# Kernel optimization log

Measured on AMD Instinct MI355X. Metric: run time of the kernel, lower is better.

Reference implementation:

```python
import jax, jax.numpy as jnp
import numpy as np

N, NFEAT, NHID, NCLASS = 384, 512, 192, 64


def setup_inputs() -> dict:
    key = jax.random.key(0)
    ks = jax.random.split(key, 16)
    s = 0.05
    inp = {
        "x": jax.random.normal(ks[0], (N, NFEAT), jnp.float32),
        # normalized dense adjacency surrogates (row-scaled so outputs stay O(1))
        "adj": jax.random.uniform(ks[1], (N, N), jnp.float32) / N,
        "adj1": jax.random.uniform(ks[2], (N, N * N), jnp.float32) / (N * N),
        # nn.Linear emb / cls
        "W_emb": jax.random.normal(ks[3], (NFEAT, NHID), jnp.float32) * s,
        "b_emb": jnp.zeros((NHID,), jnp.float32),
        "W_cls": jax.random.normal(ks[4], (NHID, NCLASS), jnp.float32) * s,
        "b_cls": jnp.zeros((NCLASS,), jnp.float32),
        # GraphConvolution gc1, gc2
        "W1": jax.random.normal(ks[5], (NHID, NHID), jnp.float32) * s,
        "b1": jnp.zeros((NHID,), jnp.float32),
        "W2": jax.random.normal(ks[6], (NHID, NHID), jnp.float32) * s,
        "b2": jnp.zeros((NHID,), jnp.float32),
        # GraphConvolution_edge gc_e, gc_e2
        "We": jax.random.normal(ks[7], (NHID, NHID), jnp.float32) * s,
        "be": jnp.zeros((NHID,), jnp.float32),
        "We2": jax.random.normal(ks[8], (NHID, NHID), jnp.float32) * s,
        "be2": jnp.zeros((NHID,), jnp.float32),
    }
    return inp


def _outer_edge(a, b):
    # [N,H] x [N,H] -> [N*N, H] elementwise outer-product edge features
    n, h = a.shape
    return (a[:, None, :] * b[None, :, :]).reshape(n * n, h)


def reference(x, adj, adj1, W_emb, b_emb, W_cls, b_cls, W1, b1, W2, b2, We, be, We2, be2):
    # eval mode: dropout is identity
    x_init = x @ W_emb + b_emb                      # [N,H]
    edge_feat = _outer_edge(x_init, x_init)          # [N*N,H]
    # gc_e: adj1 @ (edge_feat @ We) + be
    x_e = jax.nn.relu(adj1 @ (edge_feat @ We) + be)  # [N,H]
    # gc1: adj @ (x_init @ W1) + b1
    x1 = jax.nn.relu(adj @ (x_init @ W1) + b1)       # [N,H]
    xs = x1 + x_e + x_init
    x_mid = adj @ (xs @ W2) + b2                     # gc2
    edge_feat1 = _outer_edge(x1, x1)                 # [N*N,H]
    x_e2 = adj1 @ ((edge_feat + edge_feat1) @ We2) + be2  # gc_e2
    h = jax.nn.relu(x_mid + x_e2)
    logits = h @ W_cls + b_cls                       # [N,C]
    return jax.nn.log_softmax(logits, axis=1)
```

## Files before the change

### kernel.cpp

```cpp
#include <hip/hip_runtime.h>

#define NN 384
#define NF 512
#define NH 192
#define NC 64

typedef __bf16 bf16x8 __attribute__((ext_vector_type(8)));
typedef float f32x4 __attribute__((ext_vector_type(4)));

static __device__ __forceinline__ float b2f(unsigned short u) {
  union { unsigned int i; float f; } v; v.i = ((unsigned int)u) << 16; return v.f;
}
static __device__ __forceinline__ unsigned short f2b(float f) {
  unsigned int u = __float_as_uint(f);
  unsigned int r = (u + 0x7FFFu + ((u >> 16) & 1u)) >> 16;
  return (unsigned short)r;
}

__global__ void __launch_bounds__(192) k_emb(
    const float* __restrict__ x, const float* __restrict__ W_emb,
    const float* __restrict__ b_emb, const float* __restrict__ W1,
    float* __restrict__ xinit, float* __restrict__ t1,
    unsigned short* __restrict__ uT)
{
  __shared__ float xl[4][NF];
  __shared__ float xi[4][NH];
  const int r0 = blockIdx.x * 4;
  const int tid = threadIdx.x;
#pragma unroll
  for (int rr = 0; rr < 4; ++rr)
    for (int k = tid; k < NF; k += 192)
      xl[rr][k] = x[(size_t)(r0 + rr) * NF + k];
  __syncthreads();
  const int h = tid;
  float a0 = b_emb[h], a1 = a0, a2 = a0, a3 = a0;
  for (int k = 0; k < NF; ++k) {
    float w = W_emb[k * NH + h];
    a0 += xl[0][k] * w; a1 += xl[1][k] * w; a2 += xl[2][k] * w; a3 += xl[3][k] * w;
  }
  float acc[4] = {a0, a1, a2, a3};
#pragma unroll
  for (int rr = 0; rr < 4; ++rr) {
    xinit[(r0 + rr) * NH + h] = acc[rr];
    xi[rr][h] = acc[rr];
    uT[h * NN + (r0 + rr)] = f2b(acc[rr]);
  }
  __syncthreads();
  float c0 = 0.f, c1 = 0.f, c2 = 0.f, c3 = 0.f;
  for (int k = 0; k < NH; ++k) {
    float w = W1[k * NH + h];
    c0 += xi[0][k] * w; c1 += xi[1][k] * w; c2 += xi[2][k] * w; c3 += xi[3][k] * w;
  }
  t1[(r0 + 0) * NH + h] = c0;
  t1[(r0 + 1) * NH + h] = c1;
  t1[(r0 + 2) * NH + h] = c2;
  t1[(r0 + 3) * NH + h] = c3;
}

__global__ void __launch_bounds__(192) k_gc1(
    const float* __restrict__ adj, const float* __restrict__ t1,
    const float* __restrict__ b1, float* __restrict__ x1,
    unsigned short* __restrict__ vT)
{
  __shared__ float al[4][NN];
  const int r0 = blockIdx.x * 4;
  const int tid = threadIdx.x;
#pragma unroll
  for (int rr = 0; rr < 4; ++rr)
    for (int j = tid; j < NN; j += 192)
      al[rr][j] = adj[(size_t)(r0 + rr) * NN + j];
  __syncthreads();
  const int h = tid;
  float a0 = b1[h], a1 = a0, a2 = a0, a3 = a0;
  for (int j = 0; j < NN; ++j) {
    float t = t1[j * NH + h];
    a0 += al[0][j] * t; a1 += al[1][j] * t; a2 += al[2][j] * t; a3 += al[3][j] * t;
  }
  float acc[4] = {a0, a1, a2, a3};
#pragma unroll
  for (int rr = 0; rr < 4; ++rr) {
    float v = fmaxf(acc[rr], 0.f);
    x1[(r0 + rr) * NH + h] = v;
    vT[h * NN + (r0 + rr)] = f2b(v);
  }
}

__global__ void __launch_bounds__(512, 2) k_edge(
    const float* __restrict__ adj1, const unsigned short* __restrict__ uT,
    const unsigned short* __restrict__ vT,
    float* __restrict__ E0p, float* __restrict__ E1p)
{
  __shared__ __align__(16) unsigned char lds_raw[81920];
  float* Af = (float*)lds_raw;
  unsigned short* Bf = (unsigned short*)(lds_raw + 32768);

  const int tid = threadIdx.x;
  const int wv = tid >> 6, l = tid & 63;
  const int lr = l & 15, lg = l >> 4;
  const int rg = wv >> 2, hg = (wv >> 1) & 1, uv = wv & 1;
  const int bid = blockIdx.x;
  const int r = bid / 3, ig = bid - r * 3;
  const int i0 = ig * 128;
  const float* __restrict__ Ar = adj1 + (size_t)r * (NN * NN);

  const int aunit = (l & 7) ^ (l >> 3);
  const int bunit = (l & 3) ^ ((l >> 3) & 3);

  f32x4 acc[4][6];
  const f32x4 zero = {0.f, 0.f, 0.f, 0.f};
#pragma unroll
  for (int s = 0; s < 4; ++s)
#pragma unroll
    for (int t = 0; t < 6; ++t) acc[s][t] = zero;

  auto STAGE = [&](int buf, int kb) {
#pragma unroll
    for (int p = 0; p < 2; ++p) {
      const int rowbase = wv * 16 + p * 8;
      const float* g = Ar + (size_t)(i0 + rowbase + (l >> 3)) * NN + kb + 4 * aunit;
      __builtin_amdgcn_global_load_lds(
          (const __attribute__((address_space(1))) unsigned int*)g,
          (__attribute__((address_space(3))) unsigned int*)(Af + buf * 4096 + rowbase * 32),
          16, 0, 0);
    }
#pragma unroll
    for (int q = 0; q < 3; ++q) {
      const int m = wv * 3 + q;
      const int uvs = (m >= 12) ? 1 : 0;
      const int H0 = (m - uvs * 12) * 16;
      const unsigned short* src =
          (uvs ? vT : uT) + (H0 + (l >> 2)) * NN + kb + 8 * bunit;
      __builtin_amdgcn_global_load_lds(
          (const __attribute__((address_space(1))) unsigned int*)src,
          (__attribute__((address_space(3))) unsigned int*)(Bf + buf * 12288 + uvs * 6144 + H0 * 32),
          16, 0, 0);
    }
  };

  STAGE(0, 0);
  __syncthreads();

  const unsigned short* selT = uv ? vT : uT;
  int buf = 0;
  for (int kk = 0; kk < 12; ++kk) {
    if (kk < 11) STAGE(buf ^ 1, (kk + 1) * 32);

    const float* Ab = Af + buf * 4096;
    const unsigned short* Bb = Bf + buf * 12288 + uv * 6144;

    bf16x8 bfr[6];
#pragma unroll
    for (int t = 0; t < 6; ++t) {
      const int h = (hg * 6 + t) * 16 + lr;
      bfr[t] = *reinterpret_cast<const bf16x8*>(Bb + h * 32 + 8 * (lg ^ ((lr >> 1) & 3)));
    }
#pragma unroll
    for (int s = 0; s < 4; ++s) {
      const int R = rg * 64 + s * 16 + lr;
      const float* rowp = Ab + R * 32;
      f32x4 q0 = *reinterpret_cast<const f32x4*>(rowp + 4 * ((2 * lg) ^ (lr & 7)));
      f32x4 q1 = *reinterpret_cast<const f32x4*>(rowp + 4 * (((2 * lg) + 1) ^ (lr & 7)));
      bf16x8 af;
      af[0] = (__bf16)q0[0]; af[1] = (__bf16)q0[1];
      af[2] = (__bf16)q0[2]; af[3] = (__bf16)q0[3];
      af[4] = (__bf16)q1[0]; af[5] = (__bf16)q1[1];
      af[6] = (__bf16)q1[2]; af[7] = (__bf16)q1[3];
#pragma unroll
      for (int t = 0; t < 6; ++t)
        acc[s][t] = __builtin_amdgcn_mfma_f32_16x16x32_bf16(af, bfr[t], acc[s][t], 0, 0, 0);
    }
    __syncthreads();
    buf ^= 1;
  }

  float e[6];
#pragma unroll
  for (int t = 0; t < 6; ++t) {
    const int h = (hg * 6 + t) * 16 + lr;
    float ac = 0.f;
#pragma unroll
    for (int s = 0; s < 4; ++s) {
      const int ii = i0 + rg * 64 + s * 16 + lg * 4;
      ushort4 w4 = *reinterpret_cast<const ushort4*>(selT + h * NN + ii);
      ac += b2f(w4.x) * acc[s][t][0] + b2f(w4.y) * acc[s][t][1]
          + b2f(w4.z) * acc[s][t][2] + b2f(w4.w) * acc[s][t][3];
    }
    ac += __shfl_xor(ac, 16);
    ac += __shfl_xor(ac, 32);
    e[t] = ac;
  }
  float* scratch = (float*)lds_raw;
  if (rg == 1 && lg == 0) {
#pragma unroll
    for (int t = 0; t < 6; ++t)
      scratch[uv * 192 + (hg * 6 + t) * 16 + lr] = e[t];
  }
  __syncthreads();
  if (rg == 0 && lg == 0) {
    float* Ep = uv ? E1p : E0p;
#pragma unroll
    for (int t = 0; t < 6; ++t) {
      const int h = (hg * 6 + t) * 16 + lr;
      Ep[((size_t)ig * NN + r) * NH + h] = e[t] + scratch[uv * 192 + h];
    }
  }
}

__global__ void __launch_bounds__(192) k_mid(
    const float* __restrict__ E0p, const float* __restrict__ E1p,
    const float* __restrict__ x1, const float* __restrict__ xinit,
    const float* __restrict__ We, const float* __restrict__ be,
    const float* __restrict__ W2, const float* __restrict__ We2,
    const float* __restrict__ be2, float* __restrict__ t2,
    float* __restrict__ xe2)
{
  __shared__ float e0l[4][NH], s01[4][NH], xsl[4][NH];
  const int r0 = blockIdx.x * 4;
  const int h = threadIdx.x;
#pragma unroll
  for (int rr = 0; rr < 4; ++rr) {
    const int idx = (r0 + rr) * NH + h;
    float e0v = E0p[idx] + E0p[NN * NH + idx] + E0p[2 * NN * NH + idx];
    float e1v = E1p[idx] + E1p[NN * NH + idx] + E1p[2 * NN * NH + idx];
    e0l[rr][h] = e0v;
    s01[rr][h] = e0v + e1v;
  }
  __syncthreads();
  float x0 = be[h], x1a = x0, x2 = x0, x3 = x0;
  for (int k = 0; k < NH; ++k) {
    float w = We[k * NH + h];
    x0 += e0l[0][k] * w; x1a += e0l[1][k] * w; x2 += e0l[2][k] * w; x3 += e0l[3][k] * w;
  }
  float xe[4] = {x0, x1a, x2, x3};
#pragma unroll
  for (int rr = 0; rr < 4; ++rr) {
    const int idx = (r0 + rr) * NH + h;
    xsl[rr][h] = fmaxf(xe[rr], 0.f) + x1[idx] + xinit[idx];
  }
  __syncthreads();
  float t0 = 0.f, t1v = 0.f, t2v = 0.f, t3 = 0.f;
  float b0 = be2[h], b1v = b0, b2v = b0, b3 = b0;
  for (int k = 0; k < NH; ++k) {
    float w2 = W2[k * NH + h];
    float w3 = We2[k * NH + h];
    t0 += xsl[0][k] * w2; t1v += xsl[1][k] * w2; t2v += xsl[2][k] * w2; t3 += xsl[3][k] * w2;
    b0 += s01[0][k] * w3; b1v += s01[1][k] * w3; b2v += s01[2][k] * w3; b3 += s01[3][k] * w3;
  }
  t2[(r0 + 0) * NH + h] = t0;  t2[(r0 + 1) * NH + h] = t1v;
  t2[(r0 + 2) * NH + h] = t2v; t2[(r0 + 3) * NH + h] = t3;
  xe2[(r0 + 0) * NH + h] = b0;  xe2[(r0 + 1) * NH + h] = b1v;
  xe2[(r0 + 2) * NH + h] = b2v; xe2[(r0 + 3) * NH + h] = b3;
}

__global__ void __launch_bounds__(256) k_out(
    const float* __restrict__ adj, const float* __restrict__ t2,
    const float* __restrict__ b2, const float* __restrict__ xe2,
    const float* __restrict__ Wc, const float* __restrict__ bc,
    float* __restrict__ out)
{
  __shared__ float al[4][NN];
  __shared__ float hl[4][NH];
  const int r0 = blockIdx.x * 4;
  const int tid = threadIdx.x;
#pragma unroll
  for (int rr = 0; rr < 4; ++rr)
    for (int j = tid; j < NN; j += 256)
      al[rr][j] = adj[(size_t)(r0 + rr) * NN + j];
  __syncthreads();
  if (tid < NH) {
    const int h = tid;
    float a0 = b2[h], a1 = a0, a2 = a0, a3 = a0;
    for (int j = 0; j < NN; ++j) {
      float t = t2[j * NH + h];
      a0 += al[0][j] * t; a1 += al[1][j] * t; a2 += al[2][j] * t; a3 += al[3][j] * t;
    }
    float acc[4] = {a0, a1, a2, a3};
#pragma unroll
    for (int rr = 0; rr < 4; ++rr)
      hl[rr][h] = fmaxf(acc[rr] + xe2[(r0 + rr) * NH + h], 0.f);
  }
  __syncthreads();
  const int w = tid >> 6, lane = tid & 63;
  float lgt = bc[lane];
  for (int k = 0; k < NH; ++k) lgt += hl[w][k] * Wc[k * NC + lane];
  float m = lgt;
#pragma unroll
  for (int off = 32; off >= 1; off >>= 1) m = fmaxf(m, __shfl_xor(m, off));
  float s = expf(lgt - m);
#pragma unroll
  for (int off = 32; off >= 1; off >>= 1) s += __shfl_xor(s, off);
  out[(size_t)(r0 + w) * NC + lane] = lgt - m - logf(s);
}

extern "C" void kernel_launch(void* const* d_in, const int* in_sizes, int n_in,
                              void* d_out, int out_size, void* d_ws, size_t ws_size,
                              hipStream_t stream) {
  const float* x     = (const float*)d_in[0];
  const float* adj   = (const float*)d_in[1];
  const float* adj1  = (const float*)d_in[2];
  const float* W_emb = (const float*)d_in[3];
  const float* b_emb = (const float*)d_in[4];
  const float* W_cls = (const float*)d_in[5];
  const float* b_cls = (const float*)d_in[6];
  const float* W1    = (const float*)d_in[7];
  const float* b1    = (const float*)d_in[8];
  const float* W2    = (const float*)d_in[9];
  const float* b2    = (const float*)d_in[10];
  const float* We    = (const float*)d_in[11];
  const float* be    = (const float*)d_in[12];
  const float* We2   = (const float*)d_in[13];
  const float* be2   = (const float*)d_in[14];

  char* ws = (char*)d_ws;
  float* xinit = (float*)(ws + 0);
  float* t1    = (float*)(ws + 294912);
  float* x1    = (float*)(ws + 589824);
  float* E0p   = (float*)(ws + 884736);
  float* E1p   = (float*)(ws + 1769472);
  unsigned short* uT = (unsigned short*)(ws + 2654208);
  unsigned short* vT = (unsigned short*)(ws + 2801664);
  float* t2  = E0p;
  float* xe2 = E0p + NN * NH;

  k_emb<<<96, 192, 0, stream>>>(x, W_emb, b_emb, W1, xinit, t1, uT);
  k_gc1<<<96, 192, 0, stream>>>(adj, t1, b1, x1, vT);
  k_edge<<<1152, 512, 0, stream>>>(adj1, uT, vT, E0p, E1p);
  k_mid<<<96, 192, 0, stream>>>(E0p, E1p, x1, xinit, We, be, W2, We2, be2, t2, xe2);
  k_out<<<96, 256, 0, stream>>>(adj, t2, b2, xe2, W_cls, b_cls, (float*)d_out);
}
```

Baseline: 188.4 us.

## Restructure edge kernel: 64-row halves, B fragments from global, smaller LDS

The edge contraction kernel now processes two 64-row halves of its adj1 slab per block instead of one 128-row tile. Each wave owns 3 H-tiles instead of 6. The B operand (uT/vT) is loaded directly from global into registers with a one-step prefetch rather than staged through LDS. Only the fp32 adj1 tiles stay in LDS (16 KB instead of 80 KB), which lets launch bounds request 4 blocks per CU and removes the cross-wave scratch reduction. The trade-off is more global and L2 traffic for B, re-read per block, and more K iterations per block.

```diff
diff --git a/kernel.cpp b/kernel.cpp
--- a/kernel.cpp
+++ b/kernel.cpp
@@ -85,123 +85,111 @@
   }
 }
 
-__global__ void __launch_bounds__(512, 2) k_edge(
+__global__ void __launch_bounds__(512, 4) k_edge(
     const float* __restrict__ adj1, const unsigned short* __restrict__ uT,
     const unsigned short* __restrict__ vT,
     float* __restrict__ E0p, float* __restrict__ E1p)
 {
-  __shared__ __align__(16) unsigned char lds_raw[81920];
-  float* Af = (float*)lds_raw;
-  unsigned short* Bf = (unsigned short*)(lds_raw + 32768);
+  __shared__ __align__(16) float Af[2][2048];
 
   const int tid = threadIdx.x;
   const int wv = tid >> 6, l = tid & 63;
   const int lr = l & 15, lg = l >> 4;
-  const int rg = wv >> 2, hg = (wv >> 1) & 1, uv = wv & 1;
-  const int bid = blockIdx.x;
-  const int r = bid / 3, ig = bid - r * 3;
-  const int i0 = ig * 128;
+  const int hg = wv >> 1, uv = wv & 1;
+  const int r = blockIdx.x / 3, c = blockIdx.x - r * 3;
   const float* __restrict__ Ar = adj1 + (size_t)r * (NN * NN);
+  const unsigned short* __restrict__ selT = uv ? vT : uT;
 
   const int aunit = (l & 7) ^ (l >> 3);
-  const int bunit = (l & 3) ^ ((l >> 3) & 3);
-
-  f32x4 acc[4][6];
-  const f32x4 zero = {0.f, 0.f, 0.f, 0.f};
-#pragma unroll
-  for (int s = 0; s < 4; ++s)
-#pragma unroll
-    for (int t = 0; t < 6; ++t) acc[s][t] = zero;
-
-  auto STAGE = [&](int buf, int kb) {
-#pragma unroll
-    for (int p = 0; p < 2; ++p) {
-      const int rowbase = wv * 16 + p * 8;
-      const float* g = Ar + (size_t)(i0 + rowbase + (l >> 3)) * NN + kb + 4 * aunit;
-      __builtin_amdgcn_global_load_lds(
-          (const __attribute__((address_space(1))) unsigned int*)g,
-          (__attribute__((address_space(3))) unsigned int*)(Af + buf * 4096 + rowbase * 32),
-          16, 0, 0);
+
+  auto STAGE = [&](int buf, int i0h, int kb) {
+    const float* g = Ar + (size_t)(i0h + wv * 8 + (l >> 3)) * NN + kb + 4 * aunit;
+    __builtin_amdgcn_global_load_lds(
+        (const __attribute__((address_space(1))) unsigned int*)g,
+        (__attribute__((address_space(3))) unsigned int*)(&Af[buf][(wv * 8) * 32]),
+        16, 0, 0);
+  };
+
+  const unsigned short* bbase[3];
+#pragma unroll
+  for (int t = 0; t < 3; ++t)
+    bbase[t] = selT + ((hg * 3 + t) * 16 + lr) * NN + lg * 8;
+
+  bf16x8 bcur[3], bnxt[3];
+  float e[3] = {0.f, 0.f, 0.f};
+
+  STAGE(0, c * 64, 0);
+#pragma unroll
+  for (int t = 0; t < 3; ++t) bcur[t] = *reinterpret_cast<const bf16x8*>(bbase[t]);
+  __syncthreads();
+
+  int buf = 0;
+#pragma unroll
+  for (int half = 0; half < 2; ++half) {
+    const int i0h = (c + half * 3) * 64;
+    f32x4 acc[4][3];
+    const f32x4 zero = {0.f, 0.f, 0.f, 0.f};
+#pragma unroll
+    for (int s = 0; s < 4; ++s)
+#pragma unroll
+      for (int t = 0; t < 3; ++t) acc[s][t] = zero;
+
+#pragma unroll
+    for (int kk = 0; kk < 12; ++kk) {
+      const int g = half * 12 + kk;
+      if (g < 23) {
+        const int gn = g + 1;
+        const int nh = gn / 12, nk = gn - nh * 12;
+        STAGE(buf ^ 1, (c + nh * 3) * 64, nk * 32);
+#pragma unroll
+        for (int t = 0; t < 3; ++t)
+          bnxt[t] = *reinterpret_cast<const bf16x8*>(bbase[t] + nk * 32);
+      }
+#pragma unroll
+      for (int s = 0; s < 4; ++s) {
+        const int R = s * 16 + lr;
+        const float* rowp = &Af[buf][R * 32];
+        f32x4 q0 = *reinterpret_cast<const f32x4*>(rowp + 4 * ((2 * lg) ^ (lr & 7)));
+        f32x4 q1 = *reinterpret_cast<const f32x4*>(rowp + 4 * ((2 * lg + 1) ^ (lr & 7)));
+        bf16x8 af;
+        af[0] = (__bf16)q0[0]; af[1] = (__bf16)q0[1];
+        af[2] = (__bf16)q0[2]; af[3] = (__bf16)q0[3];
+        af[4] = (__bf16)q1[0]; af[5] = (__bf16)q1[1];
+        af[6] = (__bf16)q1[2]; af[7] = (__bf16)q1[3];
+#pragma unroll
+        for (int t = 0; t < 3; ++t)
+          acc[s][t] = __builtin_amdgcn_mfma_f32_16x16x32_bf16(af, bcur[t], acc[s][t], 0, 0, 0);
+      }
+      __syncthreads();
+      buf ^= 1;
+#pragma unroll
+      for (int t = 0; t < 3; ++t) bcur[t] = bnxt[t];
     }
-#pragma unroll
-    for (int q = 0; q < 3; ++q) {
-      const int m = wv * 3 + q;
-      const int uvs = (m >= 12) ? 1 : 0;
-      const int H0 = (m - uvs * 12) * 16;
-      const unsigned short* src =
-          (uvs ? vT : uT) + (H0 + (l >> 2)) * NN + kb + 8 * bunit;
-      __builtin_amdgcn_global_load_lds(
-          (const __attribute__((address_space(1))) unsigned int*)src,
-          (__attribute__((address_space(3))) unsigned int*)(Bf + buf * 12288 + uvs * 6144 + H0 * 32),
-          16, 0, 0);
+
+#pragma unroll
+    for (int t = 0; t < 3; ++t) {
+      const int h = (hg * 3 + t) * 16 + lr;
+#pragma unroll
+      for (int s = 0; s < 4; ++s) {
+        const int ii = i0h + s * 16 + lg * 4;
+        ushort4 w4 = *reinterpret_cast<const ushort4*>(selT + h * NN + ii);
+        e[t] += b2f(w4.x) * acc[s][t][0] + b2f(w4.y) * acc[s][t][1]
+              + b2f(w4.z) * acc[s][t][2] + b2f(w4.w) * acc[s][t][3];
+      }
     }
-  };
-
-  STAGE(0, 0);
-  __syncthreads();
-
-  const unsigned short* selT = uv ? vT : uT;
-  int buf = 0;
-  for (int kk = 0; kk < 12; ++kk) {
-    if (kk < 11) STAGE(buf ^ 1, (kk + 1) * 32);
-
-    const float* Ab = Af + buf * 4096;
-    const unsigned short* Bb = Bf + buf * 12288 + uv * 6144;
-
-    bf16x8 bfr[6];
-#pragma unroll
-    for (int t = 0; t < 6; ++t) {
-      const int h = (hg * 6 + t) * 16 + lr;
-      bfr[t] = *reinterpret_cast<const bf16x8*>(Bb + h * 32 + 8 * (lg ^ ((lr >> 1) & 3)));
-    }
-#pragma unroll
-    for (int s = 0; s < 4; ++s) {
-      const int R = rg * 64 + s * 16 + lr;
-      const float* rowp = Ab + R * 32;
-      f32x4 q0 = *reinterpret_cast<const f32x4*>(rowp + 4 * ((2 * lg) ^ (lr & 7)));
-      f32x4 q1 = *reinterpret_cast<const f32x4*>(rowp + 4 * (((2 * lg) + 1) ^ (lr & 7)));
-      bf16x8 af;
-      af[0] = (__bf16)q0[0]; af[1] = (__bf16)q0[1];
-      af[2] = (__bf16)q0[2]; af[3] = (__bf16)q0[3];
-      af[4] = (__bf16)q1[0]; af[5] = (__bf16)q1[1];
-      af[6] = (__bf16)q1[2]; af[7] = (__bf16)q1[3];
-#pragma unroll
-      for (int t = 0; t < 6; ++t)
-        acc[s][t] = __builtin_amdgcn_mfma_f32_16x16x32_bf16(af, bfr[t], acc[s][t], 0, 0, 0);
-    }
-    __syncthreads();
-    buf ^= 1;
-  }
-
-  float e[6];
-#pragma unroll
-  for (int t = 0; t < 6; ++t) {
-    const int h = (hg * 6 + t) * 16 + lr;
-    float ac = 0.f;
-#pragma unroll
-    for (int s = 0; s < 4; ++s) {
-      const int ii = i0 + rg * 64 + s * 16 + lg * 4;
-      ushort4 w4 = *reinterpret_cast<const ushort4*>(selT + h * NN + ii);
-      ac += b2f(w4.x) * acc[s][t][0] + b2f(w4.y) * acc[s][t][1]
-          + b2f(w4.z) * acc[s][t][2] + b2f(w4.w) * acc[s][t][3];
-    }
-    ac += __shfl_xor(ac, 16);
-    ac += __shfl_xor(ac, 32);
-    e[t] = ac;
-  }
-  float* scratch = (float*)lds_raw;
-  if (rg == 1 && lg == 0) {
-#pragma unroll
-    for (int t = 0; t < 6; ++t)
-      scratch[uv * 192 + (hg * 6 + t) * 16 + lr] = e[t];
-  }
-  __syncthreads();
-  if (rg == 0 && lg == 0) {
+  }
+
+#pragma unroll
+  for (int t = 0; t < 3; ++t) {
+    e[t] += __shfl_xor(e[t], 16);
+    e[t] += __shfl_xor(e[t], 32);
+  }
+  if (lg == 0) {
     float* Ep = uv ? E1p : E0p;
 #pragma unroll
-    for (int t = 0; t < 6; ++t) {
-      const int h = (hg * 6 + t) * 16 + lr;
-      Ep[((size_t)ig * NN + r) * NH + h] = e[t] + scratch[uv * 192 + h];
+    for (int t = 0; t < 3; ++t) {
+      const int h = (hg * 3 + t) * 16 + lr;
+      Ep[((size_t)c * NN + r) * NH + h] = e[t];
     }
   }
 }
```

After: 229.9 us. 1.22x slower.

## Load edge-kernel B operand directly from global, shrink LDS, raise occupancy

Applied to the files above, without the earlier changes.

The bf16 uT/vT operand tiles are no longer staged through LDS. Each wave now reads its B fragments straight from global memory (L2/L1) every k-step. Only the adj1 tile is kept in LDS, which cuts shared memory from 80KB to 32KB, and the launch bound is raised to allow 4 blocks per CU. The aim is more occupancy and less LDS staging traffic, at the cost of uncoalesced, latency-exposed global loads for B inside the main loop.

```diff
diff --git a/kernel.cpp b/kernel.cpp
--- a/kernel.cpp
+++ b/kernel.cpp
@@ -85,26 +85,23 @@
   }
 }
 
-__global__ void __launch_bounds__(512, 2) k_edge(
+__global__ void __launch_bounds__(512, 4) k_edge(
     const float* __restrict__ adj1, const unsigned short* __restrict__ uT,
     const unsigned short* __restrict__ vT,
     float* __restrict__ E0p, float* __restrict__ E1p)
 {
-  __shared__ __align__(16) unsigned char lds_raw[81920];
-  float* Af = (float*)lds_raw;
-  unsigned short* Bf = (unsigned short*)(lds_raw + 32768);
+  __shared__ __align__(16) float Af[2][4096];
 
   const int tid = threadIdx.x;
   const int wv = tid >> 6, l = tid & 63;
   const int lr = l & 15, lg = l >> 4;
   const int rg = wv >> 2, hg = (wv >> 1) & 1, uv = wv & 1;
-  const int bid = blockIdx.x;
-  const int r = bid / 3, ig = bid - r * 3;
+  const int r = blockIdx.x / 3, ig = blockIdx.x - r * 3;
   const int i0 = ig * 128;
   const float* __restrict__ Ar = adj1 + (size_t)r * (NN * NN);
+  const unsigned short* __restrict__ selT = uv ? vT : uT;
 
   const int aunit = (l & 7) ^ (l >> 3);
-  const int bunit = (l & 3) ^ ((l >> 3) & 3);
 
   f32x4 acc[4][6];
   const f32x4 zero = {0.f, 0.f, 0.f, 0.f};
@@ -120,46 +117,31 @@
       const float* g = Ar + (size_t)(i0 + rowbase + (l >> 3)) * NN + kb + 4 * aunit;
       __builtin_amdgcn_global_load_lds(
           (const __attribute__((address_space(1))) unsigned int*)g,
-          (__attribute__((address_space(3))) unsigned int*)(Af + buf * 4096 + rowbase * 32),
+          (__attribute__((address_space(3))) unsigned int*)(&Af[buf][rowbase * 32]),
           16, 0, 0);
     }
-#pragma unroll
-    for (int q = 0; q < 3; ++q) {
-      const int m = wv * 3 + q;
-      const int uvs = (m >= 12) ? 1 : 0;
-      const int H0 = (m - uvs * 12) * 16;
-      const unsigned short* src =
-          (uvs ? vT : uT) + (H0 + (l >> 2)) * NN + kb + 8 * bunit;
-      __builtin_amdgcn_global_load_lds(
-          (const __attribute__((address_space(1))) unsigned int*)src,
-          (__attribute__((address_space(3))) unsigned int*)(Bf + buf * 12288 + uvs * 6144 + H0 * 32),
-          16, 0, 0);
-    }
   };
 
   STAGE(0, 0);
   __syncthreads();
 
-  const unsigned short* selT = uv ? vT : uT;
   int buf = 0;
   for (int kk = 0; kk < 12; ++kk) {
     if (kk < 11) STAGE(buf ^ 1, (kk + 1) * 32);
-
-    const float* Ab = Af + buf * 4096;
-    const unsigned short* Bb = Bf + buf * 12288 + uv * 6144;
+    const int kb = kk * 32;
 
     bf16x8 bfr[6];
 #pragma unroll
-    for (int t = 0; t < 6; ++t) {
-      const int h = (hg * 6 + t) * 16 + lr;
-      bfr[t] = *reinterpret_cast<const bf16x8*>(Bb + h * 32 + 8 * (lg ^ ((lr >> 1) & 3)));
-    }
+    for (int t = 0; t < 6; ++t)
+      bfr[t] = *reinterpret_cast<const bf16x8*>(
+          selT + ((hg * 6 + t) * 16 + lr) * NN + kb + lg * 8);
+
 #pragma unroll
     for (int s = 0; s < 4; ++s) {
       const int R = rg * 64 + s * 16 + lr;
-      const float* rowp = Ab + R * 32;
+      const float* rowp = &Af[buf][R * 32];
       f32x4 q0 = *reinterpret_cast<const f32x4*>(rowp + 4 * ((2 * lg) ^ (lr & 7)));
-      f32x4 q1 = *reinterpret_cast<const f32x4*>(rowp + 4 * (((2 * lg) + 1) ^ (lr & 7)));
+      f32x4 q1 = *reinterpret_cast<const f32x4*>(rowp + 4 * ((2 * lg + 1) ^ (lr & 7)));
       bf16x8 af;
       af[0] = (__bf16)q0[0]; af[1] = (__bf16)q0[1];
       af[2] = (__bf16)q0[2]; af[3] = (__bf16)q0[3];
@@ -189,7 +171,7 @@
     ac += __shfl_xor(ac, 32);
     e[t] = ac;
   }
-  float* scratch = (float*)lds_raw;
+  float* scratch = (float*)Af;
   if (rg == 1 && lg == 0) {
 #pragma unroll
     for (int t = 0; t < 6; ++t)
```

After: 463.0 us. 2.46x slower.
